# Kernel tuning notes

Hardware: AMD Instinct MI355X
Metric: run time of the kernel (lower is better)

Reference implementation:

```python
import jax, jax.numpy as jnp
import numpy as np

B, N, G = 8, 262144, 64
EPS = 1e-6


def _log_transform(x):
    return jnp.sign(x) * jnp.log1p(jnp.abs(x))


def _group_mean_depth(points, valid, groups):
    # points: (B,N,3), valid: (B,N) bool, groups: (B,N) int in [0,G)
    z = points[..., 2]
    w = valid.astype(z.dtype)
    seg = (groups.astype(jnp.int32) + jnp.arange(B, dtype=jnp.int32)[:, None] * G).ravel()
    sums = jax.ops.segment_sum((z * w).ravel(), seg, num_segments=B * G)
    cnts = jax.ops.segment_sum(w.ravel(), seg, num_segments=B * G)
    mean = jnp.where(cnts > 0, sums / jnp.maximum(cnts, 1.0), 1.0)  # empty group -> 1.0 (skipped in torch loop)
    safe = jnp.maximum(jnp.abs(mean), EPS)
    per_point = safe[seg].reshape(z.shape)
    return jnp.where(valid, per_point, 1.0)


def _normalize_points(points, valid, groups):
    md = _group_mean_depth(points, valid, groups)
    return jnp.where(valid[..., None], points, 0.0) / md[..., None]


def _masked_mean(loss, valid):
    vm = valid if loss.ndim == valid.ndim else jnp.broadcast_to(valid[..., None], loss.shape)
    return jnp.where(vm, loss, 0.0).sum() / (vm.sum().astype(loss.dtype) + 1e-6)


def setup_inputs() -> dict:
    key = jax.random.key(0)
    ks = jax.random.split(key, 13)
    f = lambda k, s: jax.random.normal(k, s, dtype=jnp.float32)
    return {
        'pred_points': f(ks[0], (B, N, 3)),
        'target_points': f(ks[1], (B, N, 3)),
        'pred_2d': f(ks[2], (B, N, 2)),
        'target_2d': f(ks[3], (B, N, 2)),
        'pred_vis': f(ks[4], (B, N, 1)),
        'target_vis': jax.random.uniform(ks[5], (B, N), dtype=jnp.float32),
        'pred_disp': f(ks[6], (B, N, 3)),
        'target_disp': f(ks[7], (B, N, 3)),
        'pred_normal': f(ks[8], (B, N, 3)),
        'target_normal': f(ks[9], (B, N, 3)),
        'confidence': f(ks[10], (B, N, 1)),
        'mask': jax.random.randint(ks[11], (B, N), 0, 2, dtype=jnp.int32),
        'groups': jax.random.randint(ks[12], (B, N), 0, G, dtype=jnp.int32),
    }


def reference(pred_points, target_points, pred_2d, target_2d, pred_vis, target_vis,
              pred_disp, target_disp, pred_normal, target_normal, confidence, mask, groups):
    lambda_3d, lambda_raw_3d, lambda_2d = 1.0, 0.0, 0.1
    lambda_vis, lambda_disp, lambda_normal, lambda_conf = 0.1, 0.1, 0.5, 0.2
    valid = mask.astype(bool)

    # L_3D: per-group scale-invariant normalization + log transform + masked L1
    pn = _log_transform(_normalize_points(pred_points, valid, groups))
    tn = _log_transform(_normalize_points(target_points, valid, groups))
    l_3d = _masked_mean(jnp.abs(pn - tn), valid)

    # L_raw3D: raw camera-space L1 (weight 0 by default)
    l_raw3d = _masked_mean(jnp.abs(pred_points - target_points), valid)

    # L_2D
    l_2d = _masked_mean(jnp.abs(pred_2d - target_2d), valid)

    # L_vis: BCE with logits
    x = pred_vis[..., 0]
    bce = jnp.maximum(x, 0.0) - x * target_vis + jnp.log1p(jnp.exp(-jnp.abs(x)))
    l_vis = _masked_mean(bce, valid)

    # L_disp
    l_disp = _masked_mean(jnp.abs(pred_disp - target_disp), valid)

    # L_normal: 1 - cosine similarity of unit-normalized vectors
    def _unit(v):
        n = jnp.linalg.norm(v, axis=-1, keepdims=True)
        return v / jnp.maximum(n, 1e-12)
    cos = (_unit(pred_normal) * _unit(target_normal)).sum(-1)
    l_normal = _masked_mean(1.0 - cos, valid)

    # L_conf: Kendall penalty s = -log(c)
    l_conf = _masked_mean(confidence[..., 0], valid)

    return (lambda_3d * l_3d + lambda_raw_3d * l_raw3d + lambda_2d * l_2d
            + lambda_vis * l_vis + lambda_disp * l_disp
            + lambda_normal * l_normal + lambda_conf * l_conf)
```

## Files before the change

kernel.cpp:

```cpp
#include <hip/hip_runtime.h>
#include <math.h>

#define GG   64
#define NBG  512
#define TOT  2097152
#define PTS  1024
#define NBLK (TOT / PTS)

#define ZP_F   0
#define ZT_F   512
#define CNT_F  1024
#define PART_F 1536
#define WS_ZERO_BYTES (1536 * 4)

#define LN2   0.6931471805599453f
#define LOG2E 1.4426950408889634f

typedef float vf4 __attribute__((ext_vector_type(4)));
typedef int   vi4 __attribute__((ext_vector_type(4)));

__device__ __forceinline__ float fexp2(float x) { return __builtin_amdgcn_exp2f(x); }
__device__ __forceinline__ float flog2(float x) { return __builtin_amdgcn_logf(x); }
__device__ __forceinline__ float flog1p(float x) { return flog2(1.0f + x) * LN2; }

__device__ __forceinline__ float4 ntl4(const float4* p) {
    vf4 v = __builtin_nontemporal_load((const vf4*)p);
    return make_float4(v.x, v.y, v.z, v.w);
}
__device__ __forceinline__ int4 ntl4i(const int4* p) {
    vi4 v = __builtin_nontemporal_load((const vi4*)p);
    return make_int4(v.x, v.y, v.z, v.w);
}

__device__ __forceinline__ float wredf(float v) {
#pragma unroll
    for (int o = 32; o > 0; o >>= 1) v += __shfl_down(v, o, 64);
    return v;
}

__global__ __launch_bounds__(256) void k_group(const float* __restrict__ pp,
                                               const float* __restrict__ tp,
                                               const int* __restrict__ mask,
                                               const int* __restrict__ grp,
                                               float* __restrict__ ws) {
    __shared__ float4 bufA[768], bufB[768];
    __shared__ float sP[GG], sT[GG], sC[GG];
    const int tid = threadIdx.x;
    if (tid < GG) { sP[tid] = 0.f; sT[tid] = 0.f; sC[tid] = 0.f; }

    const int base = blockIdx.x * PTS;
    const int b = base >> 18;
    const int p0 = base + 4 * tid;

    const float4* gx = (const float4*)(pp + (size_t)base * 3);
    const float4* gy = (const float4*)(tp + (size_t)base * 3);
#pragma unroll
    for (int j = 0; j < 3; j++) {
        bufA[tid + 256 * j] = gx[tid + 256 * j];
        bufB[tid + 256 * j] = gy[tid + 256 * j];
    }
    const int4 M  = *(const int4*)(mask + p0);
    const int4 Gp = *(const int4*)(grp + p0);
    __syncthreads();

    float4 a0 = bufA[3 * tid], a1 = bufA[3 * tid + 1], a2 = bufA[3 * tid + 2];
    float4 b0 = bufB[3 * tid], b1 = bufB[3 * tid + 1], b2 = bufB[3 * tid + 2];
    if (M.x) { atomicAdd(&sP[Gp.x], a0.z); atomicAdd(&sT[Gp.x], b0.z); atomicAdd(&sC[Gp.x], 1.f); }
    if (M.y) { atomicAdd(&sP[Gp.y], a1.y); atomicAdd(&sT[Gp.y], b1.y); atomicAdd(&sC[Gp.y], 1.f); }
    if (M.z) { atomicAdd(&sP[Gp.z], a2.x); atomicAdd(&sT[Gp.z], b2.x); atomicAdd(&sC[Gp.z], 1.f); }
    if (M.w) { atomicAdd(&sP[Gp.w], a2.w); atomicAdd(&sT[Gp.w], b2.w); atomicAdd(&sC[Gp.w], 1.f); }
    __syncthreads();

    if (tid < GG) {
        float c = sC[tid];
        if (c != 0.0f) {
            int e = b * GG + tid;
            atomicAdd(&ws[ZP_F + e], sP[tid]);
            atomicAdd(&ws[ZT_F + e], sT[tid]);
            atomicAdd(&ws[CNT_F + e], c);
        }
    }
}

__global__ __launch_bounds__(256) void k_loss(const float* __restrict__ pp,
                                              const float* __restrict__ tp,
                                              const float* __restrict__ p2,
                                              const float* __restrict__ t2,
                                              const float* __restrict__ pv,
                                              const float* __restrict__ tv,
                                              const float* __restrict__ pd,
                                              const float* __restrict__ td,
                                              const float* __restrict__ pn,
                                              const float* __restrict__ tn,
                                              const float* __restrict__ cf,
                                              const int* __restrict__ mask,
                                              const int* __restrict__ grp,
                                              float* __restrict__ ws) {
    __shared__ float4 bufA[768], bufB[768];
    __shared__ float sPairs[2 * GG];
    const int tid = threadIdx.x;
    const int base = blockIdx.x * PTS;
    const int p0 = base + 4 * tid;
    const int b = base >> 18;

    if (tid < GG) {
        int e = b * GG + tid;
        float c = ws[CNT_F + e];
        float mP = (c > 0.f) ? ws[ZP_F + e] / fmaxf(c, 1.f) : 1.f;
        float mT = (c > 0.f) ? ws[ZT_F + e] / fmaxf(c, 1.f) : 1.f;
        sPairs[2 * tid]     = 1.f / fmaxf(fabsf(mP), 1e-6f);
        sPairs[2 * tid + 1] = 1.f / fmaxf(fabsf(mT), 1e-6f);
    }

    const int4 M  = ntl4i((const int4*)(mask + p0));
    const int4 Gp = ntl4i((const int4*)(grp + p0));
    const float w[4] = {(float)M.x, (float)M.y, (float)M.z, (float)M.w};
    const int Gs[4] = {Gp.x, Gp.y, Gp.z, Gp.w};
    __syncthreads();

    float iP[4], iT[4];
#pragma unroll
    for (int k = 0; k < 4; k++) {
        iP[k] = sPairs[2 * Gs[k]];
        iT[k] = sPairs[2 * Gs[k] + 1];
    }

    float s3d = 0.f, s2 = 0.f, sv = 0.f, sd = 0.f, sn = 0.f, sc = 0.f;

    {
        float4 Aa = ntl4(((const float4*)(p2 + 2 * (size_t)p0)) + 0);
        float4 Ab = ntl4(((const float4*)(p2 + 2 * (size_t)p0)) + 1);
        float4 Ba = ntl4(((const float4*)(t2 + 2 * (size_t)p0)) + 0);
        float4 Bb = ntl4(((const float4*)(t2 + 2 * (size_t)p0)) + 1);
        s2 = w[0] * (fabsf(Aa.x - Ba.x) + fabsf(Aa.y - Ba.y))
           + w[1] * (fabsf(Aa.z - Ba.z) + fabsf(Aa.w - Ba.w))
           + w[2] * (fabsf(Ab.x - Bb.x) + fabsf(Ab.y - Bb.y))
           + w[3] * (fabsf(Ab.z - Bb.z) + fabsf(Ab.w - Bb.w));
    }
    {
        float4 X  = ntl4((const float4*)(pv + p0));
        float4 Tg = ntl4((const float4*)(tv + p0));
        float4 C  = ntl4((const float4*)(cf + p0));
        const float xs[4] = {X.x, X.y, X.z, X.w};
        const float ts[4] = {Tg.x, Tg.y, Tg.z, Tg.w};
        const float cs[4] = {C.x, C.y, C.z, C.w};
#pragma unroll
        for (int k = 0; k < 4; k++) {
            float x = xs[k];
            float soft = flog2(1.0f + fexp2(-fabsf(x) * LOG2E)) * LN2;
            sv += w[k] * (fmaxf(x, 0.f) - x * ts[k] + soft);
            sc += w[k] * cs[k];
        }
    }

    {
        const float4* gx = (const float4*)(pp + (size_t)base * 3);
        const float4* gy = (const float4*)(tp + (size_t)base * 3);
#pragma unroll
        for (int j = 0; j < 3; j++) {
            bufA[tid + 256 * j] = ntl4(&gx[tid + 256 * j]);
            bufB[tid + 256 * j] = ntl4(&gy[tid + 256 * j]);
        }
        __syncthreads();
        float P[12], T[12];
        *(float4*)&P[0] = bufA[3 * tid]; *(float4*)&P[4] = bufA[3 * tid + 1]; *(float4*)&P[8] = bufA[3 * tid + 2];
        *(float4*)&T[0] = bufB[3 * tid]; *(float4*)&T[4] = bufB[3 * tid + 1]; *(float4*)&T[8] = bufB[3 * tid + 2];
        __syncthreads();
#pragma unroll
        for (int k = 0; k < 4; k++) {
            float acc = 0.f;
#pragma unroll
            for (int c = 0; c < 3; c++) {
                float a = P[3 * k + c] * iP[k];
                float bb = T[3 * k + c] * iT[k];
                acc += fabsf(copysignf(flog1p(fabsf(a)), a) - copysignf(flog1p(fabsf(bb)), bb));
            }
            s3d += w[k] * acc;
        }
    }
    {
        const float4* gx = (const float4*)(pd + (size_t)base * 3);
        const float4* gy = (const float4*)(td + (size_t)base * 3);
#pragma unroll
        for (int j = 0; j < 3; j++) {
            bufA[tid + 256 * j] = ntl4(&gx[tid + 256 * j]);
            bufB[tid + 256 * j] = ntl4(&gy[tid + 256 * j]);
        }
        __syncthreads();
        float P[12], T[12];
        *(float4*)&P[0] = bufA[3 * tid]; *(float4*)&P[4] = bufA[3 * tid + 1]; *(float4*)&P[8] = bufA[3 * tid + 2];
        *(float4*)&T[0] = bufB[3 * tid]; *(float4*)&T[4] = bufB[3 * tid + 1]; *(float4*)&T[8] = bufB[3 * tid + 2];
        __syncthreads();
#pragma unroll
        for (int k = 0; k < 4; k++) {
            sd += w[k] * (fabsf(P[3 * k] - T[3 * k]) + fabsf(P[3 * k + 1] - T[3 * k + 1])
                        + fabsf(P[3 * k + 2] - T[3 * k + 2]));
        }
    }
    {
        const float4* gx = (const float4*)(pn + (size_t)base * 3);
        const float4* gy = (const float4*)(tn + (size_t)base * 3);
#pragma unroll
        for (int j = 0; j < 3; j++) {
            bufA[tid + 256 * j] = ntl4(&gx[tid + 256 * j]);
            bufB[tid + 256 * j] = ntl4(&gy[tid + 256 * j]);
        }
        __syncthreads();
        float P[12], T[12];
        *(float4*)&P[0] = bufA[3 * tid]; *(float4*)&P[4] = bufA[3 * tid + 1]; *(float4*)&P[8] = bufA[3 * tid + 2];
        *(float4*)&T[0] = bufB[3 * tid]; *(float4*)&T[4] = bufB[3 * tid + 1]; *(float4*)&T[8] = bufB[3 * tid + 2];
#pragma unroll
        for (int k = 0; k < 4; k++) {
            float ax = P[3 * k], ay = P[3 * k + 1], az = P[3 * k + 2];
            float bx = T[3 * k], by = T[3 * k + 1], bz = T[3 * k + 2];
            float na = fmaf(ax, ax, fmaf(ay, ay, az * az));
            float nb = fmaf(bx, bx, fmaf(by, by, bz * bz));
            float dot = fmaf(ax, bx, fmaf(ay, by, az * bz));
            float r = __frsqrt_rn(fmaxf(na, 1e-24f)) * __frsqrt_rn(fmaxf(nb, 1e-24f));
            sn += w[k] * (1.0f - dot * r);
        }
    }

    __shared__ float sred[4][6];
    float vals[6] = {s3d, s2, sv, sd, sn, sc};
    int wid = threadIdx.x >> 6, lane = threadIdx.x & 63;
#pragma unroll
    for (int k = 0; k < 6; k++) {
        float r = wredf(vals[k]);
        if (lane == 0) sred[wid][k] = r;
    }
    __syncthreads();
    if (threadIdx.x < 6) {
        float tt = sred[0][threadIdx.x] + sred[1][threadIdx.x]
                 + sred[2][threadIdx.x] + sred[3][threadIdx.x];
        ws[PART_F + threadIdx.x * NBLK + blockIdx.x] = tt;
    }
}

__global__ __launch_bounds__(256) void k_final(const float* __restrict__ ws,
                                               float* __restrict__ out) {
    const float* part = ws + PART_F;
    double loc[6] = {0, 0, 0, 0, 0, 0};
    for (int j = threadIdx.x; j < NBLK; j += 256) {
#pragma unroll
        for (int k = 0; k < 6; k++) loc[k] += (double)part[k * NBLK + j];
    }
    float nvloc = ws[CNT_F + threadIdx.x] + ws[CNT_F + threadIdx.x + 256];

    __shared__ double dred[4][6];
    __shared__ float nred[4];
    int wid = threadIdx.x >> 6, lane = threadIdx.x & 63;
#pragma unroll
    for (int k = 0; k < 6; k++) {
        double v = loc[k];
#pragma unroll
        for (int o = 32; o > 0; o >>= 1) v += __shfl_down(v, o, 64);
        if (lane == 0) dred[wid][k] = v;
    }
    {
        float v = wredf(nvloc);
        if (lane == 0) nred[wid] = v;
    }
    __syncthreads();
    if (threadIdx.x == 0) {
        double a[6];
#pragma unroll
        for (int k = 0; k < 6; k++)
            a[k] = dred[0][k] + dred[1][k] + dred[2][k] + dred[3][k];
        double nv = (double)(nred[0] + nred[1] + nred[2] + nred[3]);
        double d1 = nv + 1e-6;
        double d3 = 3.0 * nv + 1e-6;
        double l3d   = a[0] / d3;
        double l2d   = a[1] / (2.0 * nv + 1e-6);
        double lvis  = a[2] / d1;
        double ldisp = a[3] / d3;
        double lnorm = a[4] / d1;
        double lconf = a[5] / d1;
        out[0] = (float)(l3d + 0.1 * (l2d + lvis + ldisp) + 0.5 * lnorm + 0.2 * lconf);
    }
}

extern "C" void kernel_launch(void* const* d_in, const int* in_sizes, int n_in,
                              void* d_out, int out_size, void* d_ws, size_t ws_size,
                              hipStream_t stream) {
    const float* pp = (const float*)d_in[0];
    const float* tp = (const float*)d_in[1];
    const float* p2 = (const float*)d_in[2];
    const float* t2 = (const float*)d_in[3];
    const float* pv = (const float*)d_in[4];
    const float* tv = (const float*)d_in[5];
    const float* pd = (const float*)d_in[6];
    const float* td = (const float*)d_in[7];
    const float* pn = (const float*)d_in[8];
    const float* tn = (const float*)d_in[9];
    const float* cf = (const float*)d_in[10];
    const int* mask = (const int*)d_in[11];
    const int* grp  = (const int*)d_in[12];
    float* ws = (float*)d_ws;
    float* out = (float*)d_out;

    (void)hipMemsetAsync(d_ws, 0, WS_ZERO_BYTES, stream);
    k_group<<<NBLK, 256, 0, stream>>>(pp, tp, mask, grp, ws);
    k_loss<<<NBLK, 256, 0, stream>>>(pp, tp, p2, t2, pv, tv, pd, td, pn, tn, cf, mask, grp, ws);
    k_final<<<1, 256, 0, stream>>>(ws, out);
}
```

Baseline: 79.60 us.

## Hoist loss kernel loads upfront and fuse final reduction via last-block counter

New measurement: 161.9 us. +103.4%, slower.

```diff
diff --git a/kernel.cpp b/kernel.cpp
--- a/kernel.cpp
+++ b/kernel.cpp
@@ -10,8 +10,9 @@
 #define ZP_F   0
 #define ZT_F   512
 #define CNT_F  1024
-#define PART_F 1536
-#define WS_ZERO_BYTES (1536 * 4)
+#define CTR_I  1596
+#define PART_F 1600
+#define WS_ZERO_BYTES (1600 * 4)
 
 #define LN2   0.6931471805599453f
 #define LOG2E 1.4426950408889634f
@@ -95,9 +96,15 @@
                                               const float* __restrict__ cf,
                                               const int* __restrict__ mask,
                                               const int* __restrict__ grp,
-                                              float* __restrict__ ws) {
-    __shared__ float4 bufA[768], bufB[768];
+                                              float* __restrict__ ws,
+                                              float* __restrict__ out) {
+    __shared__ float4 bufA[768], bufB[768], bufC[768], bufD[768];
     __shared__ float sPairs[2 * GG];
+    __shared__ float sred[4][6];
+    __shared__ double dred[4][6];
+    __shared__ float nred[4];
+    __shared__ int sLast;
+
     const int tid = threadIdx.x;
     const int base = blockIdx.x * PTS;
     const int p0 = base + 4 * tid;
@@ -112,12 +119,33 @@
         sPairs[2 * tid + 1] = 1.f / fmaxf(fabsf(mT), 1e-6f);
     }
 
+    {
+        const float4* g1 = (const float4*)(pp + (size_t)base * 3);
+        const float4* g2 = (const float4*)(tp + (size_t)base * 3);
+        const float4* g3 = (const float4*)(pd + (size_t)base * 3);
+        const float4* g4 = (const float4*)(td + (size_t)base * 3);
+#pragma unroll
+        for (int j = 0; j < 3; j++) {
+            bufA[tid + 256 * j] = ntl4(&g1[tid + 256 * j]);
+            bufB[tid + 256 * j] = ntl4(&g2[tid + 256 * j]);
+            bufC[tid + 256 * j] = ntl4(&g3[tid + 256 * j]);
+            bufD[tid + 256 * j] = ntl4(&g4[tid + 256 * j]);
+        }
+    }
     const int4 M  = ntl4i((const int4*)(mask + p0));
     const int4 Gp = ntl4i((const int4*)(grp + p0));
+    float4 Aa = ntl4(((const float4*)(p2 + 2 * (size_t)p0)) + 0);
+    float4 Ab = ntl4(((const float4*)(p2 + 2 * (size_t)p0)) + 1);
+    float4 Ba = ntl4(((const float4*)(t2 + 2 * (size_t)p0)) + 0);
+    float4 Bb = ntl4(((const float4*)(t2 + 2 * (size_t)p0)) + 1);
+    float4 X  = ntl4((const float4*)(pv + p0));
+    float4 Tg = ntl4((const float4*)(tv + p0));
+    float4 C  = ntl4((const float4*)(cf + p0));
+
+    __syncthreads();
+
     const float w[4] = {(float)M.x, (float)M.y, (float)M.z, (float)M.w};
     const int Gs[4] = {Gp.x, Gp.y, Gp.z, Gp.w};
-    __syncthreads();
-
     float iP[4], iT[4];
 #pragma unroll
     for (int k = 0; k < 4; k++) {
@@ -127,20 +155,11 @@
 
     float s3d = 0.f, s2 = 0.f, sv = 0.f, sd = 0.f, sn = 0.f, sc = 0.f;
 
-    {
-        float4 Aa = ntl4(((const float4*)(p2 + 2 * (size_t)p0)) + 0);
-        float4 Ab = ntl4(((const float4*)(p2 + 2 * (size_t)p0)) + 1);
-        float4 Ba = ntl4(((const float4*)(t2 + 2 * (size_t)p0)) + 0);
-        float4 Bb = ntl4(((const float4*)(t2 + 2 * (size_t)p0)) + 1);
-        s2 = w[0] * (fabsf(Aa.x - Ba.x) + fabsf(Aa.y - Ba.y))
-           + w[1] * (fabsf(Aa.z - Ba.z) + fabsf(Aa.w - Ba.w))
-           + w[2] * (fabsf(Ab.x - Bb.x) + fabsf(Ab.y - Bb.y))
-           + w[3] * (fabsf(Ab.z - Bb.z) + fabsf(Ab.w - Bb.w));
-    }
-    {
-        float4 X  = ntl4((const float4*)(pv + p0));
-        float4 Tg = ntl4((const float4*)(tv + p0));
-        float4 C  = ntl4((const float4*)(cf + p0));
+    s2 = w[0] * (fabsf(Aa.x - Ba.x) + fabsf(Aa.y - Ba.y))
+       + w[1] * (fabsf(Aa.z - Ba.z) + fabsf(Aa.w - Ba.w))
+       + w[2] * (fabsf(Ab.x - Bb.x) + fabsf(Ab.y - Bb.y))
+       + w[3] * (fabsf(Ab.z - Bb.z) + fabsf(Ab.w - Bb.w));
+    {
         const float xs[4] = {X.x, X.y, X.z, X.w};
         const float ts[4] = {Tg.x, Tg.y, Tg.z, Tg.w};
         const float cs[4] = {C.x, C.y, C.z, C.w};
@@ -152,20 +171,10 @@
             sc += w[k] * cs[k];
         }
     }
-
-    {
-        const float4* gx = (const float4*)(pp + (size_t)base * 3);
-        const float4* gy = (const float4*)(tp + (size_t)base * 3);
-#pragma unroll
-        for (int j = 0; j < 3; j++) {
-            bufA[tid + 256 * j] = ntl4(&gx[tid + 256 * j]);
-            bufB[tid + 256 * j] = ntl4(&gy[tid + 256 * j]);
-        }
-        __syncthreads();
+    {
         float P[12], T[12];
         *(float4*)&P[0] = bufA[3 * tid]; *(float4*)&P[4] = bufA[3 * tid + 1]; *(float4*)&P[8] = bufA[3 * tid + 2];
         *(float4*)&T[0] = bufB[3 * tid]; *(float4*)&T[4] = bufB[3 * tid + 1]; *(float4*)&T[8] = bufB[3 * tid + 2];
-        __syncthreads();
 #pragma unroll
         for (int k = 0; k < 4; k++) {
             float acc = 0.f;
@@ -179,31 +188,24 @@
         }
     }
     {
-        const float4* gx = (const float4*)(pd + (size_t)base * 3);
-        const float4* gy = (const float4*)(td + (size_t)base * 3);
-#pragma unroll
-        for (int j = 0; j < 3; j++) {
-            bufA[tid + 256 * j] = ntl4(&gx[tid + 256 * j]);
-            bufB[tid + 256 * j] = ntl4(&gy[tid + 256 * j]);
-        }
-        __syncthreads();
         float P[12], T[12];
-        *(float4*)&P[0] = bufA[3 * tid]; *(float4*)&P[4] = bufA[3 * tid + 1]; *(float4*)&P[8] = bufA[3 * tid + 2];
-        *(float4*)&T[0] = bufB[3 * tid]; *(float4*)&T[4] = bufB[3 * tid + 1]; *(float4*)&T[8] = bufB[3 * tid + 2];
-        __syncthreads();
+        *(float4*)&P[0] = bufC[3 * tid]; *(float4*)&P[4] = bufC[3 * tid + 1]; *(float4*)&P[8] = bufC[3 * tid + 2];
+        *(float4*)&T[0] = bufD[3 * tid]; *(float4*)&T[4] = bufD[3 * tid + 1]; *(float4*)&T[8] = bufD[3 * tid + 2];
 #pragma unroll
         for (int k = 0; k < 4; k++) {
             sd += w[k] * (fabsf(P[3 * k] - T[3 * k]) + fabsf(P[3 * k + 1] - T[3 * k + 1])
                         + fabsf(P[3 * k + 2] - T[3 * k + 2]));
         }
     }
-    {
-        const float4* gx = (const float4*)(pn + (size_t)base * 3);
-        const float4* gy = (const float4*)(tn + (size_t)base * 3);
+    __syncthreads();
+
+    {
+        const float4* g1 = (const float4*)(pn + (size_t)base * 3);
+        const float4* g2 = (const float4*)(tn + (size_t)base * 3);
 #pragma unroll
         for (int j = 0; j < 3; j++) {
-            bufA[tid + 256 * j] = ntl4(&gx[tid + 256 * j]);
-            bufB[tid + 256 * j] = ntl4(&gy[tid + 256 * j]);
+            bufA[tid + 256 * j] = ntl4(&g1[tid + 256 * j]);
+            bufB[tid + 256 * j] = ntl4(&g2[tid + 256 * j]);
         }
         __syncthreads();
         float P[12], T[12];
@@ -221,62 +223,57 @@
         }
     }
 
-    __shared__ float sred[4][6];
     float vals[6] = {s3d, s2, sv, sd, sn, sc};
-    int wid = threadIdx.x >> 6, lane = threadIdx.x & 63;
+    const int wid = tid >> 6, lane = tid & 63;
 #pragma unroll
     for (int k = 0; k < 6; k++) {
         float r = wredf(vals[k]);
         if (lane == 0) sred[wid][k] = r;
     }
     __syncthreads();
-    if (threadIdx.x < 6) {
-        float tt = sred[0][threadIdx.x] + sred[1][threadIdx.x]
-                 + sred[2][threadIdx.x] + sred[3][threadIdx.x];
-        ws[PART_F + threadIdx.x * NBLK + blockIdx.x] = tt;
-    }
-}
-
-__global__ __launch_bounds__(256) void k_final(const float* __restrict__ ws,
-                                               float* __restrict__ out) {
-    const float* part = ws + PART_F;
-    double loc[6] = {0, 0, 0, 0, 0, 0};
-    for (int j = threadIdx.x; j < NBLK; j += 256) {
-#pragma unroll
-        for (int k = 0; k < 6; k++) loc[k] += (double)part[k * NBLK + j];
-    }
-    float nvloc = ws[CNT_F + threadIdx.x] + ws[CNT_F + threadIdx.x + 256];
-
-    __shared__ double dred[4][6];
-    __shared__ float nred[4];
-    int wid = threadIdx.x >> 6, lane = threadIdx.x & 63;
-#pragma unroll
-    for (int k = 0; k < 6; k++) {
-        double v = loc[k];
-#pragma unroll
-        for (int o = 32; o > 0; o >>= 1) v += __shfl_down(v, o, 64);
-        if (lane == 0) dred[wid][k] = v;
-    }
-    {
-        float v = wredf(nvloc);
-        if (lane == 0) nred[wid] = v;
-    }
-    __syncthreads();
-    if (threadIdx.x == 0) {
-        double a[6];
-#pragma unroll
-        for (int k = 0; k < 6; k++)
-            a[k] = dred[0][k] + dred[1][k] + dred[2][k] + dred[3][k];
-        double nv = (double)(nred[0] + nred[1] + nred[2] + nred[3]);
-        double d1 = nv + 1e-6;
-        double d3 = 3.0 * nv + 1e-6;
-        double l3d   = a[0] / d3;
-        double l2d   = a[1] / (2.0 * nv + 1e-6);
-        double lvis  = a[2] / d1;
-        double ldisp = a[3] / d3;
-        double lnorm = a[4] / d1;
-        double lconf = a[5] / d1;
-        out[0] = (float)(l3d + 0.1 * (l2d + lvis + ldisp) + 0.5 * lnorm + 0.2 * lconf);
+    if (tid == 0) {
+#pragma unroll
+        for (int k = 0; k < 6; k++) {
+            float tt = sred[0][k] + sred[1][k] + sred[2][k] + sred[3][k];
+            ws[PART_F + k * NBLK + (int)blockIdx.x] = tt;
+        }
+        __threadfence();
+        int old = atomicAdd((int*)ws + CTR_I, 1);
+        sLast = (old == NBLK - 1);
+    }
+    __syncthreads();
+
+    if (sLast) {
+        __threadfence();
+        double loc[6] = {0, 0, 0, 0, 0, 0};
+        for (int j = tid; j < NBLK; j += 256) {
+#pragma unroll
+            for (int k = 0; k < 6; k++) loc[k] += (double)ws[PART_F + k * NBLK + j];
+        }
+        float nvloc = ws[CNT_F + tid] + ws[CNT_F + tid + 256];
+#pragma unroll
+        for (int k = 0; k < 6; k++) {
+            double v = loc[k];
+#pragma unroll
+            for (int o = 32; o > 0; o >>= 1) v += __shfl_down(v, o, 64);
+            if (lane == 0) dred[wid][k] = v;
+        }
+        {
+            float v = wredf(nvloc);
+            if (lane == 0) nred[wid] = v;
+        }
+        __syncthreads();
+        if (tid == 0) {
+            double a[6];
+#pragma unroll
+            for (int k = 0; k < 6; k++)
+                a[k] = dred[0][k] + dred[1][k] + dred[2][k] + dred[3][k];
+            double nv = (double)(nred[0] + nred[1] + nred[2] + nred[3]);
+            double d1 = nv + 1e-6;
+            double d3 = 3.0 * nv + 1e-6;
+            out[0] = (float)(a[0] / d3 + 0.1 * (a[1] / (2.0 * nv + 1e-6) + a[2] / d1 + a[3] / d3)
+                             + 0.5 * (a[4] / d1) + 0.2 * (a[5] / d1));
+        }
     }
 }
 
@@ -301,6 +298,5 @@
 
     (void)hipMemsetAsync(d_ws, 0, WS_ZERO_BYTES, stream);
     k_group<<<NBLK, 256, 0, stream>>>(pp, tp, mask, grp, ws);
-    k_loss<<<NBLK, 256, 0, stream>>>(pp, tp, p2, t2, pv, tv, pd, td, pn, tn, cf, mask, grp, ws);
-    k_final<<<1, 256, 0, stream>>>(ws, out);
-}
+    k_loss<<<NBLK, 256, 0, stream>>>(pp, tp, p2, t2, pv, tv, pd, td, pn, tn, cf, mask, grp, ws, out);
+}
```
